# Kernel optimization log

Measured on AMD Instinct MI355X. Metric: run time of the kernel, lower is better.

The kernel has to match this reference:

```python
import math
import jax, jax.numpy as jnp
import numpy as np

D = 2048
N = 16
B = 2
L = 4096
SCALE = math.sqrt(1.0 / float(N))


def setup_inputs() -> dict:
    key = jax.random.key(0)
    ks = jax.random.split(key, 6)
    x = jax.random.normal(ks[0], (B, D, L), dtype=jnp.float32)
    alpha = 0.2 * jax.random.normal(ks[1], (D, N, 1), dtype=jnp.float32)
    delta = 0.2 * jax.random.normal(ks[2], (D, N, 1), dtype=jnp.float32)
    theta = 0.2 * jax.random.normal(ks[3], (D, 1, 1), dtype=jnp.float32)
    gamma = jax.random.normal(ks[4], (D, N, 2), dtype=jnp.float32)
    omega = jax.random.normal(ks[5], (D,), dtype=jnp.float32)
    return {"x": x, "alpha": alpha, "delta": delta, "theta": theta,
            "gamma": gamma, "omega": omega}


def _coeffs(alpha, delta, theta, gamma):
    p = jax.nn.sigmoid(alpha)                       # (D, N, 1)
    d = jax.nn.sigmoid(delta)                       # (D, N, 1)
    wave = jnp.arange(1, N + 1, dtype=jnp.float32).reshape(1, N, 1)
    base = jax.nn.sigmoid(theta) * (2.0 * math.pi / float(N))  # (D,1,1)
    phi = wave * base                               # (D, N, 1)
    q = (1.0 - p * d).astype(jnp.complex64) * jnp.exp(1j * phi)  # (D, N, 1)
    gam = (gamma[..., 0] + 1j * gamma[..., 1]) * SCALE            # (D, N)
    return p, q, gam


def _fftconv_real(x, k):
    # x: (B, D, L), k: (D, L)  -> causal conv, keep first L samples
    n = L + L - 1
    n_fft = 1 << (n - 1).bit_length()
    X = jnp.fft.rfft(x, n=n_fft)                    # (B, D, n_fft//2+1)
    K = jnp.fft.rfft(k, n=n_fft)[None]              # (1, D, n_fft//2+1)
    y = jnp.fft.irfft(X * K, n=n_fft)[..., :L]
    return y.astype(x.dtype)


def reference(x, alpha, delta, theta, gamma, omega):
    p, q, gam = _coeffs(alpha, delta, theta, gamma)
    # kernel_d[t] = Re( sum_n p_dn * gamma_dn * q_dn^t )
    t = jnp.arange(L, dtype=jnp.float32)
    V = jnp.exp(t[None, None, :] * jnp.log(q))      # (D, N, L) = q^t
    kernel = jnp.real(jnp.sum(p * gam[..., None] * V, axis=1))  # (D, L)
    y = _fftconv_real(x, kernel) + x * omega[None, :, None]
    # last state: h_t = q * h_{t-1} + p * x_t  (hx = None)
    qs = q[..., 0]                                   # (D, N)
    ps = p[..., 0]                                   # (D, N)
    xs = jnp.moveaxis(x, -1, 0)                      # (L, B, D)
    h0 = jnp.zeros((B, D, N), dtype=jnp.complex64)

    def step(h, xt):
        # xt: (B, D); px_t = p_dn * x_t[b,d]
        h = qs[None] * h + ps[None] * xt[..., None].astype(jnp.complex64)
        return h, None

    h_last, _ = jax.lax.scan(step, h0, xs)
    h_ri = jnp.stack([h_last.real, h_last.imag], axis=-1)  # (B, D, N, 2)
    return y, h_ri
```

## Files before the change

kernel.cpp:

```cpp
#include <hip/hip_runtime.h>
#include <math.h>


constexpr int kD = 2048, kN = 16, kB = 2, kL = 4096;
constexpr int kC = 32;
constexpr int kCH = kL / kC;
constexpr int kDN = kD * kN;
constexpr float kSCALE = 0.25f;

typedef float v2 __attribute__((ext_vector_type(2)));

static __device__ __forceinline__ v2 mkv2(float a, float b) {
    v2 r; r.x = a; r.y = b; return r;
}

static __device__ __forceinline__ v2 v2fma(v2 a, v2 b, v2 c) {
#if __has_builtin(__builtin_elementwise_fma)
    return __builtin_elementwise_fma(a, b, c);
#else
    v2 r;
    r.x = __builtin_fmaf(a.x, b.x, c.x);
    r.y = __builtin_fmaf(a.y, b.y, c.y);
    return r;
#endif
}


__global__ void coeff_kernel(const float* __restrict__ alpha,
                             const float* __restrict__ delta,
                             const float* __restrict__ theta,
                             const float* __restrict__ gamma,
                             float* __restrict__ ws) {
    int i = blockIdx.x * 256 + threadIdx.x;
    if (i >= kDN) return;
    int d = i >> 4, n = i & 15;
    float p  = 1.0f / (1.0f + expf(-alpha[i]));
    float dd = 1.0f / (1.0f + expf(-delta[i]));
    float th = 1.0f / (1.0f + expf(-theta[d]));
    float phi = (float)(n + 1) * th * 0.39269908169872414f;
    float r = 1.0f - p * dd;
    float s, c;
    sincosf(phi, &s, &c);
    ws[i]           = r * c;
    ws[kDN + i]     = r * s;
    ws[2 * kDN + i] = p * kSCALE * gamma[2 * i];
    ws[3 * kDN + i] = -(p * kSCALE * gamma[2 * i + 1]);
    ws[4 * kDN + i] = p;
}

__global__ __launch_bounds__(256) void pass1_kernel(const float* __restrict__ x,
                                                    const float* __restrict__ ws,
                                                    float* __restrict__ F) {
    int tid = blockIdx.x * 256 + threadIdx.x;
    int c   = tid & (kC - 1);
    int row = tid >> 5;
    int d   = row & (kD - 1);

    const float4* q4r = (const float4*)(ws + (size_t)d * kN);
    const float4* q4i = (const float4*)(ws + kDN + (size_t)d * kN);
    float qrA[kN], qiA[kN];
#pragma unroll
    for (int k = 0; k < 4; k++) {
        float4 t0 = q4r[k];
        qrA[4*k+0]=t0.x; qrA[4*k+1]=t0.y; qrA[4*k+2]=t0.z; qrA[4*k+3]=t0.w;
        float4 t1 = q4i[k];
        qiA[4*k+0]=t1.x; qiA[4*k+1]=t1.y; qiA[4*k+2]=t1.z; qiA[4*k+3]=t1.w;
    }
    v2 qx[kN], qy[kN], u[kN];
#pragma unroll
    for (int n = 0; n < kN; n++) {
        qx[n] = mkv2(qrA[n], qrA[n]);
        qy[n] = mkv2(-qiA[n], qiA[n]);
        u[n]  = mkv2(0.0f, 0.0f);
    }

    const float4* xp = (const float4*)(x + (size_t)row * kL + (size_t)c * kCH);
#pragma unroll 1
    for (int ii = 0; ii < kCH / 32; ii++) {
        float xs[32];
#pragma unroll
        for (int k = 0; k < 8; k++) {
            float4 t = xp[ii * 8 + k];
            xs[4*k+0]=t.x; xs[4*k+1]=t.y; xs[4*k+2]=t.z; xs[4*k+3]=t.w;
        }
#pragma unroll
        for (int j = 0; j < 32; j++) {
            v2 xv = mkv2(xs[j], 0.0f);
#pragma unroll
            for (int n = 0; n < kN; n++) {
                v2 a = v2fma(qx[n], u[n], xv);
                u[n] = v2fma(qy[n], mkv2(u[n].y, u[n].x), a);
            }
        }
    }

    float4* Fp = (float4*)(F + (size_t)tid * (kN * 2));
#pragma unroll
    for (int n = 0; n < kN; n += 2)
        Fp[n >> 1] = make_float4(u[n].x, u[n].y, u[n + 1].x, u[n + 1].y);
}

__global__ void pass2_kernel(const float* __restrict__ ws,
                             float* __restrict__ FH,
                             float* __restrict__ hout) {
    int i = blockIdx.x * 256 + threadIdx.x;
    if (i >= kB * kD * kN) return;
    int n = i & 15;
    int row = i >> 4;
    int d = row & (kD - 1);
    int dn = d * kN + n;
    float qr = ws[dn], qi = ws[kDN + dn], p = ws[4 * kDN + dn];
    float ar = qr, ai = qi;
#pragma unroll
    for (int k = 0; k < 7; k++) {
        float nr = ar * ar - ai * ai;
        float ni = 2.0f * ar * ai;
        ar = nr; ai = ni;
    }
    float Hr = 0.0f, Hi = 0.0f;
    float* base = FH + (size_t)row * kC * kN * 2;
#pragma unroll 1
    for (int c = 0; c < kC; c++) {
        size_t off = ((size_t)c * kN + n) * 2;
        float Fr = base[off], Fi = base[off + 1];
        base[off] = Hr; base[off + 1] = Hi;
        float nHr = __builtin_fmaf(ar, Hr, __builtin_fmaf(-ai, Hi, Fr));
        float nHi = __builtin_fmaf(ar, Hi, __builtin_fmaf(ai, Hr, Fi));
        Hr = nHr; Hi = nHi;
    }
    hout[2 * i]     = p * Hr;
    hout[2 * i + 1] = p * Hi;
}

__global__ __launch_bounds__(256) void pass3_kernel(const float* __restrict__ x,
                                                    const float* __restrict__ ws,
                                                    const float* __restrict__ H,
                                                    const float* __restrict__ omega,
                                                    float* __restrict__ y) {
    int tid = blockIdx.x * 256 + threadIdx.x;
    int c   = tid & (kC - 1);
    int row = tid >> 5;
    int d   = row & (kD - 1);

    const float4* q4r = (const float4*)(ws + (size_t)d * kN);
    const float4* q4i = (const float4*)(ws + kDN + (size_t)d * kN);
    const float4* g4r = (const float4*)(ws + 2 * kDN + (size_t)d * kN);
    const float4* g4i = (const float4*)(ws + 3 * kDN + (size_t)d * kN);
    float qrA[kN], qiA[kN], grA[kN], giA[kN];
#pragma unroll
    for (int k = 0; k < 4; k++) {
        float4 t0 = q4r[k];
        qrA[4*k+0]=t0.x; qrA[4*k+1]=t0.y; qrA[4*k+2]=t0.z; qrA[4*k+3]=t0.w;
        float4 t1 = q4i[k];
        qiA[4*k+0]=t1.x; qiA[4*k+1]=t1.y; qiA[4*k+2]=t1.z; qiA[4*k+3]=t1.w;
        float4 t2 = g4r[k];
        grA[4*k+0]=t2.x; grA[4*k+1]=t2.y; grA[4*k+2]=t2.z; grA[4*k+3]=t2.w;
        float4 t3 = g4i[k];
        giA[4*k+0]=t3.x; giA[4*k+1]=t3.y; giA[4*k+2]=t3.z; giA[4*k+3]=t3.w;
    }
    v2 qx[kN], qy[kN], g[kN], u[kN];
#pragma unroll
    for (int n = 0; n < kN; n++) {
        qx[n] = mkv2(qrA[n], qrA[n]);
        qy[n] = mkv2(-qiA[n], qiA[n]);
        g[n]  = mkv2(grA[n], giA[n]);
    }
    const float4* Hp = (const float4*)(H + (size_t)tid * (kN * 2));
#pragma unroll
    for (int k = 0; k < kN / 2; k++) {
        float4 h = Hp[k];
        u[2 * k]     = mkv2(h.x, h.y);
        u[2 * k + 1] = mkv2(h.z, h.w);
    }
    float om = omega[d];

    const float4* xp = (const float4*)(x + (size_t)row * kL + (size_t)c * kCH);
    float4*       yp = (float4*)(y + (size_t)row * kL + (size_t)c * kCH);
#pragma unroll 1
    for (int ii = 0; ii < kCH / 32; ii++) {
        float xs[32], ys[32];
#pragma unroll
        for (int k = 0; k < 8; k++) {
            float4 t = xp[ii * 8 + k];
            xs[4*k+0]=t.x; xs[4*k+1]=t.y; xs[4*k+2]=t.z; xs[4*k+3]=t.w;
        }
#pragma unroll
        for (int j = 0; j < 32; j++) {
            v2 xv = mkv2(xs[j], 0.0f);
            v2 acc0 = mkv2(0.0f, 0.0f), acc1 = mkv2(0.0f, 0.0f);
            v2 acc2 = mkv2(0.0f, 0.0f), acc3 = mkv2(0.0f, 0.0f);
#pragma unroll
            for (int n = 0; n < kN; n += 4) {
                v2 a;
                a = v2fma(qx[n], u[n], xv);
                u[n] = v2fma(qy[n], mkv2(u[n].y, u[n].x), a);
                acc0 = v2fma(g[n], u[n], acc0);
                a = v2fma(qx[n+1], u[n+1], xv);
                u[n+1] = v2fma(qy[n+1], mkv2(u[n+1].y, u[n+1].x), a);
                acc1 = v2fma(g[n+1], u[n+1], acc1);
                a = v2fma(qx[n+2], u[n+2], xv);
                u[n+2] = v2fma(qy[n+2], mkv2(u[n+2].y, u[n+2].x), a);
                acc2 = v2fma(g[n+2], u[n+2], acc2);
                a = v2fma(qx[n+3], u[n+3], xv);
                u[n+3] = v2fma(qy[n+3], mkv2(u[n+3].y, u[n+3].x), a);
                acc3 = v2fma(g[n+3], u[n+3], acc3);
            }
            v2 s = (acc0 + acc1) + (acc2 + acc3);
            ys[j] = s.x + s.y + om * xs[j];
        }
#pragma unroll
        for (int k = 0; k < 8; k++)
            yp[ii * 8 + k] = make_float4(ys[4*k+0], ys[4*k+1], ys[4*k+2], ys[4*k+3]);
    }
}

extern "C" void kernel_launch(void* const* d_in, const int* in_sizes, int n_in,
                              void* d_out, int out_size, void* d_ws, size_t ws_size,
                              hipStream_t stream) {
    const float* x     = (const float*)d_in[0];
    const float* alpha = (const float*)d_in[1];
    const float* delta = (const float*)d_in[2];
    const float* theta = (const float*)d_in[3];
    const float* gamma = (const float*)d_in[4];
    const float* omega = (const float*)d_in[5];
    float* y    = (float*)d_out;
    float* hout = y + (size_t)kB * kD * kL;
    float* ws   = (float*)d_ws;
    float* F    = ws + 5 * (size_t)kDN;

    coeff_kernel<<<kDN / 256, 256, 0, stream>>>(alpha, delta, theta, gamma, ws);
    pass1_kernel<<<(kB * kD * kC) / 256, 256, 0, stream>>>(x, ws, F);
    pass2_kernel<<<(kB * kD * kN) / 256, 256, 0, stream>>>(ws, F, hout);
    pass3_kernel<<<(kB * kD * kC) / 256, 256, 0, stream>>>(x, ws, F, omega, y);
}
```

Measured before the change: 187.3 us.

## Rework chunked scan with fused coefficients, paired-state SIMD layout, and more chunks

The separate coefficient kernel is removed, and sigmoid/sincos coefficients are now computed inside each pass through shared memory. The complex recurrence is reorganised so each packed v2 register holds two states' real parts, or two imaginary parts, which avoids the swizzle. The chunk count can rise to 64 when workspace allows, and x loads are software-prefetched one sub-block ahead. Outputs are written with nontemporal stores. The cost is redundant transcendental work in every block, and with more chunks the sequential pass2 carries more carry traffic.

```diff
diff --git a/kernel.cpp b/kernel.cpp
--- a/kernel.cpp
+++ b/kernel.cpp
@@ -3,12 +3,10 @@
 
 
 constexpr int kD = 2048, kN = 16, kB = 2, kL = 4096;
-constexpr int kC = 32;
-constexpr int kCH = kL / kC;
-constexpr int kDN = kD * kN;
 constexpr float kSCALE = 0.25f;
 
 typedef float v2 __attribute__((ext_vector_type(2)));
+typedef float v4 __attribute__((ext_vector_type(4)));
 
 static __device__ __forceinline__ v2 mkv2(float a, float b) {
     v2 r; r.x = a; r.y = b; return r;
@@ -25,193 +23,251 @@
 #endif
 }
 
-
-__global__ void coeff_kernel(const float* __restrict__ alpha,
-                             const float* __restrict__ delta,
-                             const float* __restrict__ theta,
-                             const float* __restrict__ gamma,
-                             float* __restrict__ ws) {
-    int i = blockIdx.x * 256 + threadIdx.x;
-    if (i >= kDN) return;
-    int d = i >> 4, n = i & 15;
-    float p  = 1.0f / (1.0f + expf(-alpha[i]));
+static __device__ __forceinline__ void sigmoid_coeffs(
+        const float* __restrict__ alpha, const float* __restrict__ delta,
+        const float* __restrict__ theta, int d, int n,
+        float& qr, float& qi, float& p) {
+    int i = d * kN + n;
+    p        = 1.0f / (1.0f + expf(-alpha[i]));
     float dd = 1.0f / (1.0f + expf(-delta[i]));
     float th = 1.0f / (1.0f + expf(-theta[d]));
     float phi = (float)(n + 1) * th * 0.39269908169872414f;
     float r = 1.0f - p * dd;
     float s, c;
     sincosf(phi, &s, &c);
-    ws[i]           = r * c;
-    ws[kDN + i]     = r * s;
-    ws[2 * kDN + i] = p * kSCALE * gamma[2 * i];
-    ws[3 * kDN + i] = -(p * kSCALE * gamma[2 * i + 1]);
-    ws[4 * kDN + i] = p;
-}
-
-__global__ __launch_bounds__(256) void pass1_kernel(const float* __restrict__ x,
-                                                    const float* __restrict__ ws,
-                                                    float* __restrict__ F) {
-    int tid = blockIdx.x * 256 + threadIdx.x;
-    int c   = tid & (kC - 1);
-    int row = tid >> 5;
-    int d   = row & (kD - 1);
-
-    const float4* q4r = (const float4*)(ws + (size_t)d * kN);
-    const float4* q4i = (const float4*)(ws + kDN + (size_t)d * kN);
-    float qrA[kN], qiA[kN];
-#pragma unroll
-    for (int k = 0; k < 4; k++) {
-        float4 t0 = q4r[k];
-        qrA[4*k+0]=t0.x; qrA[4*k+1]=t0.y; qrA[4*k+2]=t0.z; qrA[4*k+3]=t0.w;
-        float4 t1 = q4i[k];
-        qiA[4*k+0]=t1.x; qiA[4*k+1]=t1.y; qiA[4*k+2]=t1.z; qiA[4*k+3]=t1.w;
-    }
-    v2 qx[kN], qy[kN], u[kN];
-#pragma unroll
-    for (int n = 0; n < kN; n++) {
-        qx[n] = mkv2(qrA[n], qrA[n]);
-        qy[n] = mkv2(-qiA[n], qiA[n]);
-        u[n]  = mkv2(0.0f, 0.0f);
-    }
-
-    const float4* xp = (const float4*)(x + (size_t)row * kL + (size_t)c * kCH);
+    qr = r * c;
+    qi = r * s;
+}
+
+
+template <int C>
+__global__ __launch_bounds__(256) void pass1_kernel(
+        const float* __restrict__ x,
+        const float* __restrict__ alpha, const float* __restrict__ delta,
+        const float* __restrict__ theta, float* __restrict__ F) {
+    constexpr int CH = kL / C;
+    constexpr int RPB = 256 / C;
+    constexpr int NSI = CH / 16;
+    __shared__ float qrS[RPB][kN], qiS[RPB][kN];
+
+    int t = threadIdx.x;
+    int row0 = blockIdx.x * RPB;
+    if (t < RPB * kN) {
+        int lr = t / kN, n = t % kN;
+        int d = (row0 + lr) & (kD - 1);
+        float qr, qi, p;
+        sigmoid_coeffs(alpha, delta, theta, d, n, qr, qi, p);
+        qrS[lr][n] = qr;
+        qiS[lr][n] = qi;
+    }
+    __syncthreads();
+
+    int lr = t / C, c = t % C;
+    int row = row0 + lr;
+    v2 qr[8], qi[8], ur[8], vi[8];
+    const v2* qrp = (const v2*)qrS[lr];
+    const v2* qip = (const v2*)qiS[lr];
+#pragma unroll
+    for (int j = 0; j < 8; j++) {
+        qr[j] = qrp[j]; qi[j] = qip[j];
+        ur[j] = mkv2(0.0f, 0.0f); vi[j] = mkv2(0.0f, 0.0f);
+    }
+
+    const float4* xp = (const float4*)(x + (size_t)row * kL + (size_t)c * CH);
+    float4 buf[4];
+#pragma unroll
+    for (int k = 0; k < 4; k++) buf[k] = xp[k];
 #pragma unroll 1
-    for (int ii = 0; ii < kCH / 32; ii++) {
-        float xs[32];
-#pragma unroll
-        for (int k = 0; k < 8; k++) {
-            float4 t = xp[ii * 8 + k];
-            xs[4*k+0]=t.x; xs[4*k+1]=t.y; xs[4*k+2]=t.z; xs[4*k+3]=t.w;
-        }
-#pragma unroll
-        for (int j = 0; j < 32; j++) {
-            v2 xv = mkv2(xs[j], 0.0f);
-#pragma unroll
-            for (int n = 0; n < kN; n++) {
-                v2 a = v2fma(qx[n], u[n], xv);
-                u[n] = v2fma(qy[n], mkv2(u[n].y, u[n].x), a);
+    for (int ii = 0; ii < NSI; ii++) {
+        int nb = (ii + 1 < NSI) ? ii + 1 : ii;
+        float4 nxt[4];
+#pragma unroll
+        for (int k = 0; k < 4; k++) nxt[k] = xp[nb * 4 + k];
+        float xs[16];
+#pragma unroll
+        for (int k = 0; k < 4; k++) {
+            xs[4*k+0]=buf[k].x; xs[4*k+1]=buf[k].y; xs[4*k+2]=buf[k].z; xs[4*k+3]=buf[k].w;
+        }
+#pragma unroll
+        for (int jstep = 0; jstep < 16; jstep++) {
+            v2 xx = mkv2(xs[jstep], xs[jstep]);
+#pragma unroll
+            for (int j = 0; j < 8; j++) {
+                v2 s = qi[j] * ur[j];
+                v2 tt = v2fma(qr[j], ur[j], xx);
+                ur[j] = v2fma(qi[j], vi[j], tt);
+                vi[j] = v2fma(qr[j], vi[j], -s);
             }
         }
-    }
-
-    float4* Fp = (float4*)(F + (size_t)tid * (kN * 2));
-#pragma unroll
-    for (int n = 0; n < kN; n += 2)
-        Fp[n >> 1] = make_float4(u[n].x, u[n].y, u[n + 1].x, u[n + 1].y);
-}
-
-__global__ void pass2_kernel(const float* __restrict__ ws,
+#pragma unroll
+        for (int k = 0; k < 4; k++) buf[k] = nxt[k];
+    }
+
+    float4* Fp = (float4*)(F + ((size_t)row * C + c) * 32);
+#pragma unroll
+    for (int j = 0; j < 8; j++)
+        Fp[j] = make_float4(ur[j].x, ur[j].y, vi[j].x, vi[j].y);
+}
+
+template <int C>
+__global__ void pass2_kernel(const float* __restrict__ alpha,
+                             const float* __restrict__ delta,
+                             const float* __restrict__ theta,
                              float* __restrict__ FH,
                              float* __restrict__ hout) {
-    int i = blockIdx.x * 256 + threadIdx.x;
-    if (i >= kB * kD * kN) return;
-    int n = i & 15;
-    int row = i >> 4;
-    int d = row & (kD - 1);
-    int dn = d * kN + n;
-    float qr = ws[dn], qi = ws[kDN + dn], p = ws[4 * kDN + dn];
-    float ar = qr, ai = qi;
-#pragma unroll
-    for (int k = 0; k < 7; k++) {
-        float nr = ar * ar - ai * ai;
-        float ni = 2.0f * ar * ai;
-        ar = nr; ai = ni;
-    }
-    float Hr = 0.0f, Hi = 0.0f;
-    float* base = FH + (size_t)row * kC * kN * 2;
+    constexpr int CH = kL / C;
+    constexpr int LOG = (CH == 64) ? 6 : 7;
+    int idx = blockIdx.x * 256 + threadIdx.x;
+    if (idx >= kB * kD * 8) return;
+    int j = idx & 7, row = idx >> 3, d = row & (kD - 1);
+    float a0r, a0i, p0, a1r, a1i, p1;
+    sigmoid_coeffs(alpha, delta, theta, d, 2 * j,     a0r, a0i, p0);
+    sigmoid_coeffs(alpha, delta, theta, d, 2 * j + 1, a1r, a1i, p1);
+#pragma unroll
+    for (int k = 0; k < LOG; k++) {
+        float n0r = a0r * a0r - a0i * a0i, n0i = 2.0f * a0r * a0i;
+        float n1r = a1r * a1r - a1i * a1i, n1i = 2.0f * a1r * a1i;
+        a0r = n0r; a0i = n0i; a1r = n1r; a1i = n1i;
+    }
+    float H0r = 0.0f, H0i = 0.0f, H1r = 0.0f, H1i = 0.0f;
+    float* base = FH + (size_t)row * C * 32 + j * 4;
 #pragma unroll 1
-    for (int c = 0; c < kC; c++) {
-        size_t off = ((size_t)c * kN + n) * 2;
-        float Fr = base[off], Fi = base[off + 1];
-        base[off] = Hr; base[off + 1] = Hi;
-        float nHr = __builtin_fmaf(ar, Hr, __builtin_fmaf(-ai, Hi, Fr));
-        float nHi = __builtin_fmaf(ar, Hi, __builtin_fmaf(ai, Hr, Fi));
-        Hr = nHr; Hi = nHi;
-    }
-    hout[2 * i]     = p * Hr;
-    hout[2 * i + 1] = p * Hi;
-}
-
-__global__ __launch_bounds__(256) void pass3_kernel(const float* __restrict__ x,
-                                                    const float* __restrict__ ws,
-                                                    const float* __restrict__ H,
-                                                    const float* __restrict__ omega,
-                                                    float* __restrict__ y) {
-    int tid = blockIdx.x * 256 + threadIdx.x;
-    int c   = tid & (kC - 1);
-    int row = tid >> 5;
-    int d   = row & (kD - 1);
-
-    const float4* q4r = (const float4*)(ws + (size_t)d * kN);
-    const float4* q4i = (const float4*)(ws + kDN + (size_t)d * kN);
-    const float4* g4r = (const float4*)(ws + 2 * kDN + (size_t)d * kN);
-    const float4* g4i = (const float4*)(ws + 3 * kDN + (size_t)d * kN);
-    float qrA[kN], qiA[kN], grA[kN], giA[kN];
-#pragma unroll
-    for (int k = 0; k < 4; k++) {
-        float4 t0 = q4r[k];
-        qrA[4*k+0]=t0.x; qrA[4*k+1]=t0.y; qrA[4*k+2]=t0.z; qrA[4*k+3]=t0.w;
-        float4 t1 = q4i[k];
-        qiA[4*k+0]=t1.x; qiA[4*k+1]=t1.y; qiA[4*k+2]=t1.z; qiA[4*k+3]=t1.w;
-        float4 t2 = g4r[k];
-        grA[4*k+0]=t2.x; grA[4*k+1]=t2.y; grA[4*k+2]=t2.z; grA[4*k+3]=t2.w;
-        float4 t3 = g4i[k];
-        giA[4*k+0]=t3.x; giA[4*k+1]=t3.y; giA[4*k+2]=t3.z; giA[4*k+3]=t3.w;
-    }
-    v2 qx[kN], qy[kN], g[kN], u[kN];
-#pragma unroll
-    for (int n = 0; n < kN; n++) {
-        qx[n] = mkv2(qrA[n], qrA[n]);
-        qy[n] = mkv2(-qiA[n], qiA[n]);
-        g[n]  = mkv2(grA[n], giA[n]);
-    }
-    const float4* Hp = (const float4*)(H + (size_t)tid * (kN * 2));
-#pragma unroll
-    for (int k = 0; k < kN / 2; k++) {
-        float4 h = Hp[k];
-        u[2 * k]     = mkv2(h.x, h.y);
-        u[2 * k + 1] = mkv2(h.z, h.w);
-    }
-    float om = omega[d];
-
-    const float4* xp = (const float4*)(x + (size_t)row * kL + (size_t)c * kCH);
-    float4*       yp = (float4*)(y + (size_t)row * kL + (size_t)c * kCH);
+    for (int c = 0; c < C; c++) {
+        float4 f = *(float4*)(base + (size_t)c * 32);
+        float F0r = f.x, F1r = f.y, F0i = -f.z, F1i = -f.w;
+        *(float4*)(base + (size_t)c * 32) = make_float4(H0r, H1r, -H0i, -H1i);
+        float n0r = __builtin_fmaf(a0r, H0r, __builtin_fmaf(-a0i, H0i, F0r));
+        float n0i = __builtin_fmaf(a0r, H0i, __builtin_fmaf( a0i, H0r, F0i));
+        float n1r = __builtin_fmaf(a1r, H1r, __builtin_fmaf(-a1i, H1i, F1r));
+        float n1i = __builtin_fmaf(a1r, H1i, __builtin_fmaf( a1i, H1r, F1i));
+        H0r = n0r; H0i = n0i; H1r = n1r; H1i = n1i;
+    }
+    float4* hp = (float4*)(hout + (size_t)row * 32 + j * 4);
+    *hp = make_float4(p0 * H0r, p0 * H0i, p1 * H1r, p1 * H1i);
+}
+
+template <int C>
+__global__ __launch_bounds__(256) void pass3_kernel(
+        const float* __restrict__ x,
+        const float* __restrict__ alpha, const float* __restrict__ delta,
+        const float* __restrict__ theta, const float* __restrict__ gamma,
+        const float* __restrict__ omega,
+        const float* __restrict__ H, float* __restrict__ y) {
+    constexpr int CH = kL / C;
+    constexpr int RPB = 256 / C;
+    constexpr int NSI = CH / 16;
+    __shared__ float qrS[RPB][kN], qiS[RPB][kN], grS[RPB][kN], gvS[RPB][kN];
+    __shared__ float omS[RPB];
+
+    int t = threadIdx.x;
+    int row0 = blockIdx.x * RPB;
+    if (t < RPB * kN) {
+        int lr = t / kN, n = t % kN;
+        int d = (row0 + lr) & (kD - 1);
+        float qr, qi, p;
+        sigmoid_coeffs(alpha, delta, theta, d, n, qr, qi, p);
+        int i = d * kN + n;
+        qrS[lr][n] = qr;
+        qiS[lr][n] = qi;
+        grS[lr][n] = p * kSCALE * gamma[2 * i];
+        gvS[lr][n] = p * kSCALE * gamma[2 * i + 1];
+        if (n == 0) omS[lr] = omega[d];
+    }
+    __syncthreads();
+
+    int lr = t / C, c = t % C;
+    int row = row0 + lr;
+    v2 qr[8], qi[8], gr[8], gv[8], ur[8], vi[8];
+    {
+        const v2* qrp = (const v2*)qrS[lr];
+        const v2* qip = (const v2*)qiS[lr];
+        const v2* grp = (const v2*)grS[lr];
+        const v2* gvp = (const v2*)gvS[lr];
+#pragma unroll
+        for (int j = 0; j < 8; j++) {
+            qr[j] = qrp[j]; qi[j] = qip[j]; gr[j] = grp[j]; gv[j] = gvp[j];
+        }
+    }
+    const float4* Hp = (const float4*)(H + ((size_t)row * C + c) * 32);
+#pragma unroll
+    for (int j = 0; j < 8; j++) {
+        float4 h = Hp[j];
+        ur[j] = mkv2(h.x, h.y);
+        vi[j] = mkv2(h.z, h.w);
+    }
+    float om = omS[lr];
+
+    const float4* xp = (const float4*)(x + (size_t)row * kL + (size_t)c * CH);
+    v4*           yp = (v4*)(y + (size_t)row * kL + (size_t)c * CH);
+    float4 buf[4];
+#pragma unroll
+    for (int k = 0; k < 4; k++) buf[k] = xp[k];
 #pragma unroll 1
-    for (int ii = 0; ii < kCH / 32; ii++) {
-        float xs[32], ys[32];
-#pragma unroll
-        for (int k = 0; k < 8; k++) {
-            float4 t = xp[ii * 8 + k];
-            xs[4*k+0]=t.x; xs[4*k+1]=t.y; xs[4*k+2]=t.z; xs[4*k+3]=t.w;
-        }
-#pragma unroll
-        for (int j = 0; j < 32; j++) {
-            v2 xv = mkv2(xs[j], 0.0f);
-            v2 acc0 = mkv2(0.0f, 0.0f), acc1 = mkv2(0.0f, 0.0f);
-            v2 acc2 = mkv2(0.0f, 0.0f), acc3 = mkv2(0.0f, 0.0f);
-#pragma unroll
-            for (int n = 0; n < kN; n += 4) {
-                v2 a;
-                a = v2fma(qx[n], u[n], xv);
-                u[n] = v2fma(qy[n], mkv2(u[n].y, u[n].x), a);
-                acc0 = v2fma(g[n], u[n], acc0);
-                a = v2fma(qx[n+1], u[n+1], xv);
-                u[n+1] = v2fma(qy[n+1], mkv2(u[n+1].y, u[n+1].x), a);
-                acc1 = v2fma(g[n+1], u[n+1], acc1);
-                a = v2fma(qx[n+2], u[n+2], xv);
-                u[n+2] = v2fma(qy[n+2], mkv2(u[n+2].y, u[n+2].x), a);
-                acc2 = v2fma(g[n+2], u[n+2], acc2);
-                a = v2fma(qx[n+3], u[n+3], xv);
-                u[n+3] = v2fma(qy[n+3], mkv2(u[n+3].y, u[n+3].x), a);
-                acc3 = v2fma(g[n+3], u[n+3], acc3);
+    for (int ii = 0; ii < NSI; ii++) {
+        int nb = (ii + 1 < NSI) ? ii + 1 : ii;
+        float4 nxt[4];
+#pragma unroll
+        for (int k = 0; k < 4; k++) nxt[k] = xp[nb * 4 + k];
+        float xs[16], ys[16];
+#pragma unroll
+        for (int k = 0; k < 4; k++) {
+            xs[4*k+0]=buf[k].x; xs[4*k+1]=buf[k].y; xs[4*k+2]=buf[k].z; xs[4*k+3]=buf[k].w;
+        }
+#pragma unroll
+        for (int jstep = 0; jstep < 16; jstep++) {
+            v2 xx = mkv2(xs[jstep], xs[jstep]);
+            v2 a0 = mkv2(0.0f, 0.0f), a1 = mkv2(0.0f, 0.0f);
+            v2 a2 = mkv2(0.0f, 0.0f), a3 = mkv2(0.0f, 0.0f);
+#pragma unroll
+            for (int j = 0; j < 8; j += 4) {
+                v2 s, tt;
+                s = qi[j] * ur[j];
+                tt = v2fma(qr[j], ur[j], xx);
+                ur[j] = v2fma(qi[j], vi[j], tt);
+                vi[j] = v2fma(qr[j], vi[j], -s);
+                a0 = v2fma(gr[j], ur[j], a0);
+                a0 = v2fma(gv[j], vi[j], a0);
+                s = qi[j+1] * ur[j+1];
+                tt = v2fma(qr[j+1], ur[j+1], xx);
+                ur[j+1] = v2fma(qi[j+1], vi[j+1], tt);
+                vi[j+1] = v2fma(qr[j+1], vi[j+1], -s);
+                a1 = v2fma(gr[j+1], ur[j+1], a1);
+                a1 = v2fma(gv[j+1], vi[j+1], a1);
+                s = qi[j+2] * ur[j+2];
+                tt = v2fma(qr[j+2], ur[j+2], xx);
+                ur[j+2] = v2fma(qi[j+2], vi[j+2], tt);
+                vi[j+2] = v2fma(qr[j+2], vi[j+2], -s);
+                a2 = v2fma(gr[j+2], ur[j+2], a2);
+                a2 = v2fma(gv[j+2], vi[j+2], a2);
+                s = qi[j+3] * ur[j+3];
+                tt = v2fma(qr[j+3], ur[j+3], xx);
+                ur[j+3] = v2fma(qi[j+3], vi[j+3], tt);
+                vi[j+3] = v2fma(qr[j+3], vi[j+3], -s);
+                a3 = v2fma(gr[j+3], ur[j+3], a3);
+                a3 = v2fma(gv[j+3], vi[j+3], a3);
             }
-            v2 s = (acc0 + acc1) + (acc2 + acc3);
-            ys[j] = s.x + s.y + om * xs[j];
-        }
-#pragma unroll
-        for (int k = 0; k < 8; k++)
-            yp[ii * 8 + k] = make_float4(ys[4*k+0], ys[4*k+1], ys[4*k+2], ys[4*k+3]);
-    }
+            v2 sm = (a0 + a1) + (a2 + a3);
+            ys[jstep] = sm.x + sm.y + om * xs[jstep];
+        }
+#pragma unroll
+        for (int k = 0; k < 4; k++) {
+            v4 o;
+            o.x = ys[4*k+0]; o.y = ys[4*k+1]; o.z = ys[4*k+2]; o.w = ys[4*k+3];
+            __builtin_nontemporal_store(o, yp + ii * 4 + k);
+        }
+#pragma unroll
+        for (int k = 0; k < 4; k++) buf[k] = nxt[k];
+    }
+}
+
+template <int C>
+static void launch_all(const float* x, const float* alpha, const float* delta,
+                       const float* theta, const float* gamma, const float* omega,
+                       float* y, float* hout, float* F, hipStream_t stream) {
+    pass1_kernel<C><<<(kB * kD * C) / 256, 256, 0, stream>>>(x, alpha, delta, theta, F);
+    pass2_kernel<C><<<(kB * kD * 8 + 255) / 256, 256, 0, stream>>>(alpha, delta, theta, F, hout);
+    pass3_kernel<C><<<(kB * kD * C) / 256, 256, 0, stream>>>(x, alpha, delta, theta,
+                                                             gamma, omega, F, y);
 }
 
 extern "C" void kernel_launch(void* const* d_in, const int* in_sizes, int n_in,
@@ -225,11 +281,11 @@
     const float* omega = (const float*)d_in[5];
     float* y    = (float*)d_out;
     float* hout = y + (size_t)kB * kD * kL;
-    float* ws   = (float*)d_ws;
-    float* F    = ws + 5 * (size_t)kDN;
-
-    coeff_kernel<<<kDN / 256, 256, 0, stream>>>(alpha, delta, theta, gamma, ws);
-    pass1_kernel<<<(kB * kD * kC) / 256, 256, 0, stream>>>(x, ws, F);
-    pass2_kernel<<<(kB * kD * kN) / 256, 256, 0, stream>>>(ws, F, hout);
-    pass3_kernel<<<(kB * kD * kC) / 256, 256, 0, stream>>>(x, ws, F, omega, y);
-}
+    float* F    = (float*)d_ws;
+
+    size_t need64 = (size_t)kB * kD * 64 * 32 * sizeof(float);
+    if (ws_size >= need64)
+        launch_all<64>(x, alpha, delta, theta, gamma, omega, y, hout, F, stream);
+    else
+        launch_all<32>(x, alpha, delta, theta, gamma, omega, y, hout, F, stream);
+}
```

Result: slower. 324.7 us (+73.4%).

## Fuse coefficient, chunk-scan and output passes into one kernel with in-wave prefix scan

Applied to the files above, without the earlier changes.

Replaces the four-kernel pipeline (coefficients, per-chunk partial states, serial carry pass, output pass) with a single kernel. Each block handles two rows, and each wave handles half a row. x is staged once in padded shared memory. Chunk carries are combined with a shuffle-based parallel prefix scan over complex powers of q instead of a global-memory carry pass. Each lane pair splits the 16 modes in half, which cuts register pressure. This removes the second global read of x, the F workspace round trip and three launches, at the cost of a log-depth scan and shuffle reductions.

```diff
diff --git a/kernel.cpp b/kernel.cpp
--- a/kernel.cpp
+++ b/kernel.cpp
@@ -3,233 +3,198 @@
 
 
 constexpr int kD = 2048, kN = 16, kB = 2, kL = 4096;
-constexpr int kC = 32;
-constexpr int kCH = kL / kC;
-constexpr int kDN = kD * kN;
+constexpr int kRows = kB * kD;
 constexpr float kSCALE = 0.25f;
-
-typedef float v2 __attribute__((ext_vector_type(2)));
-
-static __device__ __forceinline__ v2 mkv2(float a, float b) {
-    v2 r; r.x = a; r.y = b; return r;
-}
-
-static __device__ __forceinline__ v2 v2fma(v2 a, v2 b, v2 c) {
-#if __has_builtin(__builtin_elementwise_fma)
-    return __builtin_elementwise_fma(a, b, c);
-#else
-    v2 r;
-    r.x = __builtin_fmaf(a.x, b.x, c.x);
-    r.y = __builtin_fmaf(a.y, b.y, c.y);
-    return r;
-#endif
-}
-
-
-__global__ void coeff_kernel(const float* __restrict__ alpha,
-                             const float* __restrict__ delta,
-                             const float* __restrict__ theta,
-                             const float* __restrict__ gamma,
-                             float* __restrict__ ws) {
-    int i = blockIdx.x * 256 + threadIdx.x;
-    if (i >= kDN) return;
-    int d = i >> 4, n = i & 15;
-    float p  = 1.0f / (1.0f + expf(-alpha[i]));
-    float dd = 1.0f / (1.0f + expf(-delta[i]));
-    float th = 1.0f / (1.0f + expf(-theta[d]));
+constexpr int kXS = 33;
+
+__global__ __launch_bounds__(256, 4) void ema_kernel(
+    const float* __restrict__ x, const float* __restrict__ alpha,
+    const float* __restrict__ delta, const float* __restrict__ theta,
+    const float* __restrict__ gamma, const float* __restrict__ omega,
+    float* __restrict__ y, float* __restrict__ hout) {
+
+  __shared__ float xs[4][64 * kXS];
+  __shared__ float coeff[4][88];
+  __shared__ float btot[2][32];
+
+  const int tid = threadIdx.x;
+  const int wave = tid >> 6, lane = tid & 63;
+  const int rowL = wave >> 1, w = wave & 1;
+  const int row = blockIdx.x * 2 + rowL;
+  const int d = row & (kD - 1);
+  const int cL = lane >> 1, half = lane & 1;
+
+  if (lane < kN) {
+    int n = lane, i = d * kN + n;
+    float p  = 1.f / (1.f + expf(-alpha[i]));
+    float dd = 1.f / (1.f + expf(-delta[i]));
+    float th = 1.f / (1.f + expf(-theta[d]));
     float phi = (float)(n + 1) * th * 0.39269908169872414f;
-    float r = 1.0f - p * dd;
+    float r = 1.f - p * dd;
     float s, c;
     sincosf(phi, &s, &c);
-    ws[i]           = r * c;
-    ws[kDN + i]     = r * s;
-    ws[2 * kDN + i] = p * kSCALE * gamma[2 * i];
-    ws[3 * kDN + i] = -(p * kSCALE * gamma[2 * i + 1]);
-    ws[4 * kDN + i] = p;
-}
-
-__global__ __launch_bounds__(256) void pass1_kernel(const float* __restrict__ x,
-                                                    const float* __restrict__ ws,
-                                                    float* __restrict__ F) {
-    int tid = blockIdx.x * 256 + threadIdx.x;
-    int c   = tid & (kC - 1);
-    int row = tid >> 5;
-    int d   = row & (kD - 1);
-
-    const float4* q4r = (const float4*)(ws + (size_t)d * kN);
-    const float4* q4i = (const float4*)(ws + kDN + (size_t)d * kN);
-    float qrA[kN], qiA[kN];
+    coeff[wave][n]      = r * c;
+    coeff[wave][16 + n] = -r * s;
+    coeff[wave][32 + n] = p * kSCALE * gamma[2 * i];
+    coeff[wave][48 + n] = p * kSCALE * gamma[2 * i + 1];
+    coeff[wave][64 + n] = p;
+    if (n == 0) coeff[wave][80] = omega[d];
+  }
+
+  {
+    const float4* xp = (const float4*)(x + (size_t)row * kL + w * 2048);
+#pragma unroll
+    for (int m = 0; m < 8; m++) {
+      float4 t = xp[m * 64 + lane];
+      int cc = 4 * m + (lane >> 4);
+      int jb = 4 * (lane & 15);
+      xs[wave][(jb + 0) * kXS + cc] = t.x;
+      xs[wave][(jb + 1) * kXS + cc] = t.y;
+      xs[wave][(jb + 2) * kXS + cc] = t.z;
+      xs[wave][(jb + 3) * kXS + cc] = t.w;
+    }
+  }
+  __syncthreads();
+
+  float qr[8], qv[8];
+#pragma unroll
+  for (int m = 0; m < 8; m++) {
+    qr[m] = coeff[wave][8 * half + m];
+    qv[m] = coeff[wave][16 + 8 * half + m];
+  }
+
+  float ur[8], uv[8];
+#pragma unroll
+  for (int m = 0; m < 8; m++) { ur[m] = 0.f; uv[m] = 0.f; }
+#pragma unroll 1
+  for (int j0 = 0; j0 < 64; j0 += 16) {
+#pragma unroll
+    for (int jj = 0; jj < 16; jj++) {
+      float xv = xs[wave][(j0 + jj) * kXS + cL];
+#pragma unroll
+      for (int m = 0; m < 8; m++) {
+        float nr = fmaf(qr[m], ur[m], fmaf(-qv[m], uv[m], xv));
+        float nv = fmaf(qr[m], uv[m], qv[m] * ur[m]);
+        ur[m] = nr; uv[m] = nv;
+      }
+    }
+  }
+
+  float Ar[8], Av[8];
+#pragma unroll
+  for (int m = 0; m < 8; m++) { Ar[m] = qr[m]; Av[m] = qv[m]; }
+#pragma unroll
+  for (int k = 0; k < 6; k++) {
+#pragma unroll
+    for (int m = 0; m < 8; m++) {
+      float t = Ar[m] * Ar[m] - Av[m] * Av[m];
+      Av[m] = 2.f * Ar[m] * Av[m];
+      Ar[m] = t;
+    }
+  }
+#pragma unroll
+  for (int dd = 1; dd <= 16; dd <<= 1) {
+    bool act = (cL >= dd);
+#pragma unroll
+    for (int m = 0; m < 8; m++) {
+      float oBr = __shfl_up(ur[m], 2 * dd, 64);
+      float oBv = __shfl_up(uv[m], 2 * dd, 64);
+      float oAr = __shfl_up(Ar[m], 2 * dd, 64);
+      float oAv = __shfl_up(Av[m], 2 * dd, 64);
+      if (act) {
+        ur[m] = fmaf(Ar[m], oBr, fmaf(-Av[m], oBv, ur[m]));
+        uv[m] = fmaf(Ar[m], oBv, fmaf(Av[m], oBr, uv[m]));
+        float t = Ar[m] * oAr - Av[m] * oAv;
+        Av[m] = fmaf(Ar[m], oAv, Av[m] * oAr);
+        Ar[m] = t;
+      }
+    }
+  }
+  if (w == 0 && cL == 31) {
+#pragma unroll
+    for (int m = 0; m < 8; m++) {
+      btot[rowL][(8 * half + m) * 2]     = ur[m];
+      btot[rowL][(8 * half + m) * 2 + 1] = uv[m];
+    }
+  }
+  __syncthreads();
+  float tr[8], tv[8];
+#pragma unroll
+  for (int m = 0; m < 8; m++) { tr[m] = 0.f; tv[m] = 0.f; }
+  if (w == 1) {
+#pragma unroll
+    for (int m = 0; m < 8; m++) {
+      tr[m] = btot[rowL][(8 * half + m) * 2];
+      tv[m] = btot[rowL][(8 * half + m) * 2 + 1];
+    }
+#pragma unroll
+    for (int m = 0; m < 8; m++) {
+      float nr = fmaf(Ar[m], tr[m], fmaf(-Av[m], tv[m], ur[m]));
+      float nv = fmaf(Ar[m], tv[m], fmaf(Av[m], tr[m], uv[m]));
+      ur[m] = nr; uv[m] = nv;
+    }
+  }
+  if (w == 1 && cL == 31) {
+    float4* hp = (float4*)(hout + (size_t)row * 32 + half * 16);
 #pragma unroll
     for (int k = 0; k < 4; k++) {
-        float4 t0 = q4r[k];
-        qrA[4*k+0]=t0.x; qrA[4*k+1]=t0.y; qrA[4*k+2]=t0.z; qrA[4*k+3]=t0.w;
-        float4 t1 = q4i[k];
-        qiA[4*k+0]=t1.x; qiA[4*k+1]=t1.y; qiA[4*k+2]=t1.z; qiA[4*k+3]=t1.w;
-    }
-    v2 qx[kN], qy[kN], u[kN];
-#pragma unroll
-    for (int n = 0; n < kN; n++) {
-        qx[n] = mkv2(qrA[n], qrA[n]);
-        qy[n] = mkv2(-qiA[n], qiA[n]);
-        u[n]  = mkv2(0.0f, 0.0f);
-    }
-
-    const float4* xp = (const float4*)(x + (size_t)row * kL + (size_t)c * kCH);
+      int m0 = 2 * k, m1 = 2 * k + 1;
+      float p0 = coeff[wave][64 + 8 * half + m0];
+      float p1 = coeff[wave][64 + 8 * half + m1];
+      hp[k] = make_float4(p0 * ur[m0], -p0 * uv[m0], p1 * ur[m1], -p1 * uv[m1]);
+    }
+  }
+#pragma unroll
+  for (int m = 0; m < 8; m++) {
+    float hr = __shfl_up(ur[m], 2, 64);
+    float hv = __shfl_up(uv[m], 2, 64);
+    if (cL == 0) { hr = (w == 1) ? tr[m] : 0.f; hv = (w == 1) ? tv[m] : 0.f; }
+    ur[m] = hr; uv[m] = hv;
+  }
+
+  float gr[8], gv[8];
+#pragma unroll
+  for (int m = 0; m < 8; m++) {
+    gr[m] = coeff[wave][32 + 8 * half + m];
+    gv[m] = coeff[wave][48 + 8 * half + m];
+  }
+  float om = coeff[wave][80];
+  float* ybase = y + (size_t)row * kL + (size_t)(w * 32 + cL) * 64 + half * 8;
+  float buf[8];
 #pragma unroll 1
-    for (int ii = 0; ii < kCH / 32; ii++) {
-        float xs[32];
-#pragma unroll
-        for (int k = 0; k < 8; k++) {
-            float4 t = xp[ii * 8 + k];
-            xs[4*k+0]=t.x; xs[4*k+1]=t.y; xs[4*k+2]=t.z; xs[4*k+3]=t.w;
-        }
-#pragma unroll
-        for (int j = 0; j < 32; j++) {
-            v2 xv = mkv2(xs[j], 0.0f);
-#pragma unroll
-            for (int n = 0; n < kN; n++) {
-                v2 a = v2fma(qx[n], u[n], xv);
-                u[n] = v2fma(qy[n], mkv2(u[n].y, u[n].x), a);
-            }
-        }
-    }
-
-    float4* Fp = (float4*)(F + (size_t)tid * (kN * 2));
-#pragma unroll
-    for (int n = 0; n < kN; n += 2)
-        Fp[n >> 1] = make_float4(u[n].x, u[n].y, u[n + 1].x, u[n + 1].y);
-}
-
-__global__ void pass2_kernel(const float* __restrict__ ws,
-                             float* __restrict__ FH,
-                             float* __restrict__ hout) {
-    int i = blockIdx.x * 256 + threadIdx.x;
-    if (i >= kB * kD * kN) return;
-    int n = i & 15;
-    int row = i >> 4;
-    int d = row & (kD - 1);
-    int dn = d * kN + n;
-    float qr = ws[dn], qi = ws[kDN + dn], p = ws[4 * kDN + dn];
-    float ar = qr, ai = qi;
-#pragma unroll
-    for (int k = 0; k < 7; k++) {
-        float nr = ar * ar - ai * ai;
-        float ni = 2.0f * ar * ai;
-        ar = nr; ai = ni;
-    }
-    float Hr = 0.0f, Hi = 0.0f;
-    float* base = FH + (size_t)row * kC * kN * 2;
-#pragma unroll 1
-    for (int c = 0; c < kC; c++) {
-        size_t off = ((size_t)c * kN + n) * 2;
-        float Fr = base[off], Fi = base[off + 1];
-        base[off] = Hr; base[off + 1] = Hi;
-        float nHr = __builtin_fmaf(ar, Hr, __builtin_fmaf(-ai, Hi, Fr));
-        float nHi = __builtin_fmaf(ar, Hi, __builtin_fmaf(ai, Hr, Fi));
-        Hr = nHr; Hi = nHi;
-    }
-    hout[2 * i]     = p * Hr;
-    hout[2 * i + 1] = p * Hi;
-}
-
-__global__ __launch_bounds__(256) void pass3_kernel(const float* __restrict__ x,
-                                                    const float* __restrict__ ws,
-                                                    const float* __restrict__ H,
-                                                    const float* __restrict__ omega,
-                                                    float* __restrict__ y) {
-    int tid = blockIdx.x * 256 + threadIdx.x;
-    int c   = tid & (kC - 1);
-    int row = tid >> 5;
-    int d   = row & (kD - 1);
-
-    const float4* q4r = (const float4*)(ws + (size_t)d * kN);
-    const float4* q4i = (const float4*)(ws + kDN + (size_t)d * kN);
-    const float4* g4r = (const float4*)(ws + 2 * kDN + (size_t)d * kN);
-    const float4* g4i = (const float4*)(ws + 3 * kDN + (size_t)d * kN);
-    float qrA[kN], qiA[kN], grA[kN], giA[kN];
-#pragma unroll
-    for (int k = 0; k < 4; k++) {
-        float4 t0 = q4r[k];
-        qrA[4*k+0]=t0.x; qrA[4*k+1]=t0.y; qrA[4*k+2]=t0.z; qrA[4*k+3]=t0.w;
-        float4 t1 = q4i[k];
-        qiA[4*k+0]=t1.x; qiA[4*k+1]=t1.y; qiA[4*k+2]=t1.z; qiA[4*k+3]=t1.w;
-        float4 t2 = g4r[k];
-        grA[4*k+0]=t2.x; grA[4*k+1]=t2.y; grA[4*k+2]=t2.z; grA[4*k+3]=t2.w;
-        float4 t3 = g4i[k];
-        giA[4*k+0]=t3.x; giA[4*k+1]=t3.y; giA[4*k+2]=t3.z; giA[4*k+3]=t3.w;
-    }
-    v2 qx[kN], qy[kN], g[kN], u[kN];
-#pragma unroll
-    for (int n = 0; n < kN; n++) {
-        qx[n] = mkv2(qrA[n], qrA[n]);
-        qy[n] = mkv2(-qiA[n], qiA[n]);
-        g[n]  = mkv2(grA[n], giA[n]);
-    }
-    const float4* Hp = (const float4*)(H + (size_t)tid * (kN * 2));
-#pragma unroll
-    for (int k = 0; k < kN / 2; k++) {
-        float4 h = Hp[k];
-        u[2 * k]     = mkv2(h.x, h.y);
-        u[2 * k + 1] = mkv2(h.z, h.w);
-    }
-    float om = omega[d];
-
-    const float4* xp = (const float4*)(x + (size_t)row * kL + (size_t)c * kCH);
-    float4*       yp = (float4*)(y + (size_t)row * kL + (size_t)c * kCH);
-#pragma unroll 1
-    for (int ii = 0; ii < kCH / 32; ii++) {
-        float xs[32], ys[32];
-#pragma unroll
-        for (int k = 0; k < 8; k++) {
-            float4 t = xp[ii * 8 + k];
-            xs[4*k+0]=t.x; xs[4*k+1]=t.y; xs[4*k+2]=t.z; xs[4*k+3]=t.w;
-        }
-#pragma unroll
-        for (int j = 0; j < 32; j++) {
-            v2 xv = mkv2(xs[j], 0.0f);
-            v2 acc0 = mkv2(0.0f, 0.0f), acc1 = mkv2(0.0f, 0.0f);
-            v2 acc2 = mkv2(0.0f, 0.0f), acc3 = mkv2(0.0f, 0.0f);
-#pragma unroll
-            for (int n = 0; n < kN; n += 4) {
-                v2 a;
-                a = v2fma(qx[n], u[n], xv);
-                u[n] = v2fma(qy[n], mkv2(u[n].y, u[n].x), a);
-                acc0 = v2fma(g[n], u[n], acc0);
-                a = v2fma(qx[n+1], u[n+1], xv);
-                u[n+1] = v2fma(qy[n+1], mkv2(u[n+1].y, u[n+1].x), a);
-                acc1 = v2fma(g[n+1], u[n+1], acc1);
-                a = v2fma(qx[n+2], u[n+2], xv);
-                u[n+2] = v2fma(qy[n+2], mkv2(u[n+2].y, u[n+2].x), a);
-                acc2 = v2fma(g[n+2], u[n+2], acc2);
-                a = v2fma(qx[n+3], u[n+3], xv);
-                u[n+3] = v2fma(qy[n+3], mkv2(u[n+3].y, u[n+3].x), a);
-                acc3 = v2fma(g[n+3], u[n+3], acc3);
-            }
-            v2 s = (acc0 + acc1) + (acc2 + acc3);
-            ys[j] = s.x + s.y + om * xs[j];
-        }
-#pragma unroll
-        for (int k = 0; k < 8; k++)
-            yp[ii * 8 + k] = make_float4(ys[4*k+0], ys[4*k+1], ys[4*k+2], ys[4*k+3]);
-    }
+  for (int j0 = 0; j0 < 64; j0 += 16) {
+#pragma unroll
+    for (int jj = 0; jj < 16; jj++) {
+      float xv = xs[wave][(j0 + jj) * kXS + cL];
+      float acc = 0.f;
+#pragma unroll
+      for (int m = 0; m < 8; m++) {
+        float nr = fmaf(qr[m], ur[m], fmaf(-qv[m], uv[m], xv));
+        float nv = fmaf(qr[m], uv[m], qv[m] * ur[m]);
+        ur[m] = nr; uv[m] = nv;
+        acc = fmaf(gr[m], nr, fmaf(gv[m], nv, acc));
+      }
+      float ytot = acc + __shfl_xor(acc, 1, 64);
+      ytot = fmaf(om, xv, ytot);
+      if ((jj & 8) == half * 8) buf[jj & 7] = ytot;
+    }
+    float4* yp = (float4*)(ybase + j0);
+    yp[0] = make_float4(buf[0], buf[1], buf[2], buf[3]);
+    yp[1] = make_float4(buf[4], buf[5], buf[6], buf[7]);
+  }
 }
 
 extern "C" void kernel_launch(void* const* d_in, const int* in_sizes, int n_in,
                               void* d_out, int out_size, void* d_ws, size_t ws_size,
                               hipStream_t stream) {
-    const float* x     = (const float*)d_in[0];
-    const float* alpha = (const float*)d_in[1];
-    const float* delta = (const float*)d_in[2];
-    const float* theta = (const float*)d_in[3];
-    const float* gamma = (const float*)d_in[4];
-    const float* omega = (const float*)d_in[5];
-    float* y    = (float*)d_out;
-    float* hout = y + (size_t)kB * kD * kL;
-    float* ws   = (float*)d_ws;
-    float* F    = ws + 5 * (size_t)kDN;
-
-    coeff_kernel<<<kDN / 256, 256, 0, stream>>>(alpha, delta, theta, gamma, ws);
-    pass1_kernel<<<(kB * kD * kC) / 256, 256, 0, stream>>>(x, ws, F);
-    pass2_kernel<<<(kB * kD * kN) / 256, 256, 0, stream>>>(ws, F, hout);
-    pass3_kernel<<<(kB * kD * kC) / 256, 256, 0, stream>>>(x, ws, F, omega, y);
+  const float* x     = (const float*)d_in[0];
+  const float* alpha = (const float*)d_in[1];
+  const float* delta = (const float*)d_in[2];
+  const float* theta = (const float*)d_in[3];
+  const float* gamma = (const float*)d_in[4];
+  const float* omega = (const float*)d_in[5];
+  float* y    = (float*)d_out;
+  float* hout = y + (size_t)kB * kD * kL;
+  ema_kernel<<<kRows / 2, 256, 0, stream>>>(x, alpha, delta, theta, gamma,
+                                            omega, y, hout);
 }
```

After: 416.3 us. 122% more time.
